# Optimization experiments

Hardware: AMD Instinct MI355X
Metric: run time of the kernel (lower is better)

## Reference

```python
import jax, jax.numpy as jnp
import numpy as np

B, L, K, NRBF = 2, 2048, 32, 16
NODE_F, EDGE_F = 128, 128
MAX_REL = 32  # af2 relpos -> 2*32+1 = 65 bins
NODE_IN, EDGE_IN = 21 + 6 + 8, 65 + 25 * NRBF + 1 + 2


def _ln(x, g, b, eps=1e-5):
    mu = jnp.mean(x, -1, keepdims=True)
    var = jnp.var(x, -1, keepdims=True)
    return (x - mu) / jnp.sqrt(var + eps) * g + b


def _normalize(t):
    return jnp.nan_to_num(t / jnp.linalg.norm(t, axis=-1, keepdims=True))


def _dihedral(p0, p1, p2, p3):
    u0, u1, u2 = p2 - p1, p0 - p1, p3 - p2
    n1 = _normalize(jnp.cross(u0, u1))
    n2 = _normalize(jnp.cross(u0, u2))
    sgn = jnp.sign(jnp.sum(jnp.cross(u1, u2) * u0, -1))
    return jnp.nan_to_num(sgn * jnp.arccos(jnp.sum(n1 * n2, -1)))


def setup_inputs() -> dict:
    key = jax.random.key(0)
    ks = jax.random.split(key, 9)
    return {
        "X": jax.random.normal(ks[0], (B, L, 4, 3), jnp.float32) * 5.0,
        "S": jax.random.randint(ks[1], (B, L), 0, 21),
        "BB_D_sincos": jax.random.normal(ks[2], (B, L, 3, 2), jnp.float32),
        "SC_D_sincos": jax.random.normal(ks[3], (B, L, 4, 2), jnp.float32),
        "chain_indices": jax.random.randint(ks[4], (B, L), 0, 2),
        "mask": jnp.ones((B, L), jnp.float32),
        "W_node": jax.random.normal(ks[5], (NODE_IN, NODE_F), jnp.float32) * 0.05,
        "b_node": jnp.zeros((NODE_F,), jnp.float32),
        "g_node": jnp.ones((NODE_F,), jnp.float32),
        "beta_node": jnp.zeros((NODE_F,), jnp.float32),
        "W_edge": jax.random.normal(ks[6], (EDGE_IN, EDGE_F), jnp.float32) * 0.05,
        "b_edge": jnp.zeros((EDGE_F,), jnp.float32),
        "g_edge": jnp.ones((EDGE_F,), jnp.float32),
        "beta_edge": jnp.zeros((EDGE_F,), jnp.float32),
    }


def reference(X, S, BB_D_sincos, SC_D_sincos, chain_indices, mask,
              W_node, b_node, g_node, beta_node,
              W_edge, b_edge, g_edge, beta_edge):
    Bn, Ln = X.shape[:2]
    N, Ca, C, O = X[:, :, 0], X[:, :, 1], X[:, :, 2], X[:, :, 3]
    # ---- masked pairwise Ca distances + kNN topk (smallest) ----
    m2 = mask[:, None, :] * mask[:, :, None]                      # [B,L,L]
    dX = Ca[:, :, None, :] - Ca[:, None, :, :]
    D = m2 * jnp.sqrt(jnp.sum(dX * dX, -1) + 1e-6)
    D_adj = D + 2.0 * (1.0 - m2) * jnp.max(D, -1, keepdims=True)
    _, E_idx = jax.lax.top_k(-D_adj, K)                           # [B,L,K]
    bidx = jnp.arange(Bn)[:, None, None]
    # ---- af2 relative-position one-hot (residue_index=None path) ----
    offset = E_idx - jnp.arange(Ln)[None, :, None]
    E_pos = jax.nn.one_hot(jnp.clip(offset + MAX_REL, 0, 2 * MAX_REL),
                           2 * MAX_REL + 1, dtype=jnp.float32)    # [B,L,K,65]
    # ---- impute CB, 5x5 atomic-distance RBFs at neighbors only ----
    bv, cv = Ca - N, C - Ca
    Cb = -0.58273431 * jnp.cross(bv, cv) + 0.56802827 * bv - 0.54067466 * cv + Ca
    X5 = jnp.stack((N, Ca, C, O, Cb), axis=-2)                    # [B,L,5,3]
    X5_nb = X5[bidx, E_idx]                                       # [B,L,K,5,3]
    dA = X5[:, :, None, :, None, :] - X5_nb[:, :, :, None, :, :]  # [B,L,K,5i,5j,3]
    Dn = jnp.sqrt(jnp.sum(dA * dA, -1) + 1e-6)                    # [B,L,K,5,5]
    mu = jnp.linspace(0.0, 20.0, NRBF)
    sigma = 20.0 / NRBF
    RBF_all = jnp.exp(-(((Dn[..., None] - mu) / sigma) ** 2))
    RBF_all = RBF_all.reshape(Bn, Ln, K, 25 * NRBF)               # i-major, j, rbf order
    # ---- edge type: same-chain indicator + 1 ----
    ch_nb = chain_indices[bidx, E_idx]
    E_type = ((ch_nb == chain_indices[:, :, None]).astype(jnp.float32) + 1.0)[..., None]
    # ---- pairwise dihedrals, evaluated only at neighbors ----
    N_nb, Ca_nb, C_nb = N[bidx, E_idx], Ca[bidx, E_idx], C[bidx, E_idx]
    ir_phi = _dihedral(C[:, :, None, :], N_nb, Ca_nb, C_nb)
    ir_psi = _dihedral(N[:, :, None, :], Ca[:, :, None, :], C[:, :, None, :], N_nb)
    dihed = jnp.stack((ir_phi, ir_psi), -1)                       # [B,L,K,2]
    # ---- fuse + embed ----
    E = jnp.concatenate((E_pos, RBF_all, E_type, dihed), -1)      # [B,L,K,468]
    V = jnp.concatenate((jax.nn.one_hot(S, 21, dtype=jnp.float32),
                         BB_D_sincos.reshape(Bn, Ln, -1),
                         SC_D_sincos.reshape(Bn, Ln, -1)), -1)    # [B,L,35]
    h_V = _ln(V @ W_node + b_node, g_node, beta_node)
    h_E = _ln(E @ W_edge + b_edge, g_edge, beta_edge)
    return (h_V, h_E, E_idx, X)
```

## Files before the change

### kernel.cpp

```cpp
#include <hip/hip_runtime.h>
#include <math.h>

#define NB 2
#define NL 2048
#define NK 32
#define NODE_F 128
#define EDGE_F 128

#define OFF_HV   0
#define OFF_HE   (NB*NL*NODE_F)
#define OFF_EIDX (OFF_HE + NB*NL*NK*EDGE_F)
#define OFF_X    (OFF_EIDX + NB*NL*NK)

#define ACH 7
#define BCH 6
#define SAW 232

typedef __attribute__((ext_vector_type(8))) short v8s;
typedef __attribute__((ext_vector_type(4))) float v4f;

__device__ __forceinline__ short f2bf(float f) {
    unsigned u = __float_as_uint(f);
    unsigned r = u + 0x7fffu + ((u >> 16) & 1u);
    return (short)(r >> 16);
}

#if __has_builtin(__builtin_amdgcn_exp2f)
#define EXP2F(x) __builtin_amdgcn_exp2f(x)
#else
#define EXP2F(x) __expf((x) * 0.6931471805599453f)
#endif

__device__ __forceinline__ unsigned bfpack(float f0, float f1) {
    unsigned u0 = __float_as_uint(f0), u1 = __float_as_uint(f1);
#if __has_builtin(__builtin_amdgcn_perm)
    return __builtin_amdgcn_perm(u1, u0, 0x07060302u);
#else
    return (u1 & 0xFFFF0000u) | (u0 >> 16);
#endif
}

template<int CTRL>
__device__ __forceinline__ unsigned long long dpp_min_step(unsigned long long x) {
    unsigned lo = (unsigned)x, hi = (unsigned)(x >> 32);
    unsigned plo = (unsigned)__builtin_amdgcn_update_dpp((int)lo, (int)lo, CTRL, 0xF, 0xF, false);
    unsigned phi = (unsigned)__builtin_amdgcn_update_dpp((int)hi, (int)hi, CTRL, 0xF, 0xF, false);
    unsigned long long p = (((unsigned long long)phi) << 32) | plo;
    return p < x ? p : x;
}
__device__ __forceinline__ unsigned long long wave_min_u64_dpp(unsigned long long x) {
    x = dpp_min_step<0xB1>(x);
    x = dpp_min_step<0x4E>(x);
    x = dpp_min_step<0x141>(x);
    x = dpp_min_step<0x140>(x);
    x = dpp_min_step<0x142>(x);
    x = dpp_min_step<0x143>(x);
    return x;
}

__device__ __forceinline__ void cross3(const float a[3], const float b[3], float c[3]) {
    c[0] = a[1]*b[2] - a[2]*b[1];
    c[1] = a[2]*b[0] - a[0]*b[2];
    c[2] = a[0]*b[1] - a[1]*b[0];
}
__device__ __forceinline__ float dot3(const float a[3], const float b[3]) {
    return a[0]*b[0] + a[1]*b[1] + a[2]*b[2];
}
__device__ float dihedral_f(const float p0[3], const float p1[3],
                            const float p2[3], const float p3[3]) {
    float u0[3], u1[3], u2[3];
    for (int d = 0; d < 3; d++) {
        u0[d] = p2[d] - p1[d];
        u1[d] = p0[d] - p1[d];
        u2[d] = p3[d] - p2[d];
    }
    float n1[3], n2[3], c12[3];
    cross3(u0, u1, n1);
    cross3(u0, u2, n2);
    cross3(u1, u2, c12);
    float l1 = sqrtf(dot3(n1, n1));
    float l2 = sqrtf(dot3(n2, n2));
    float cosang = dot3(n1, n2) / (l1 * l2);
    float s = dot3(c12, u0);
    float sgn = (s > 0.f) ? 1.f : ((s < 0.f) ? -1.f : 0.f);
    float r = sgn * acosf(cosang);
    return isnan(r) ? 0.f : r;
}

__global__ void prep_wconv_kernel(const float* __restrict__ X, float* __restrict__ X5,
                                  float* __restrict__ Cax, float* __restrict__ Cay,
                                  float* __restrict__ Caz, float* __restrict__ out,
                                  const float* __restrict__ We, const float* __restrict__ be,
                                  short* __restrict__ WTf) {
    int blk = blockIdx.x;
    if (blk < 16) {
        int row = blk * 256 + threadIdx.x;
        float v[12];
#pragma unroll
        for (int t = 0; t < 12; t++) v[t] = X[row * 12 + t];
#pragma unroll
        for (int t = 0; t < 12; t++) out[OFF_X + row * 12 + t] = v[t];
        Cax[row] = v[3]; Cay[row] = v[4]; Caz[row] = v[5];
        float bv[3], cv[3], cr[3];
        for (int d = 0; d < 3; d++) { bv[d] = v[3+d] - v[d]; cv[d] = v[6+d] - v[3+d]; }
        cross3(bv, cv, cr);
        float* x5 = X5 + row * 15;
#pragma unroll
        for (int t = 0; t < 12; t++) x5[t] = v[t];
        for (int d = 0; d < 3; d++)
            x5[12 + d] = -0.58273431f * cr[d] + 0.56802827f * bv[d] - 0.54067466f * cv[d] + v[3+d];
    } else {
        int t = (blk - 16) * 256 + threadIdx.x;
        if (t >= 13 * 8 * 64) return;
        int lane = t & 63;
        int nt = (t >> 6) & 7;
        int ch = t >> 9;
        int n = nt * 16 + (lane & 15);
        int kbase = ch * 32 + (lane >> 4) * 8;
        short* dst = WTf + (size_t)t * 8;
#pragma unroll
        for (int j = 0; j < 8; j++) {
            int k = kbase + j;
            float f;
            if (k < 403) f = We[(65 + k) * 128 + n];
            else if (k == 403) f = be[n];
            else f = 0.f;
            dst[j] = f2bf(f);
        }
    }
}

#define KNN_QMIN(Q) {                                                                  \
    unsigned long long a_ = key[(Q)*8+0] < key[(Q)*8+1] ? key[(Q)*8+0] : key[(Q)*8+1]; \
    unsigned long long b_ = key[(Q)*8+2] < key[(Q)*8+3] ? key[(Q)*8+2] : key[(Q)*8+3]; \
    unsigned long long c_ = key[(Q)*8+4] < key[(Q)*8+5] ? key[(Q)*8+4] : key[(Q)*8+5]; \
    unsigned long long d_ = key[(Q)*8+6] < key[(Q)*8+7] ? key[(Q)*8+6] : key[(Q)*8+7]; \
    a_ = a_ < b_ ? a_ : b_; c_ = c_ < d_ ? c_ : d_;                                    \
    qm[(Q)] = a_ < c_ ? a_ : c_; }

#define KNN_STEP(Q) {                                                                  \
    _Pragma("unroll")                                                                  \
    for (int i_ = 0; i_ < 8; i_++)                                                     \
        key[(Q)*8+i_] = (me && tstar == (Q)*8+i_) ? ~0ull : key[(Q)*8+i_];             \
    KNN_QMIN(Q) }

__global__ __launch_bounds__(256) void knn_node_kernel(const float* __restrict__ Cax,
                                                       const float* __restrict__ Cay,
                                                       const float* __restrict__ Caz,
                                                       const float* __restrict__ mask,
                                                       const int* __restrict__ S,
                                                       const float* __restrict__ BB,
                                                       const float* __restrict__ SC,
                                                       const float* __restrict__ Wn,
                                                       const float* __restrict__ bn,
                                                       const float* __restrict__ gn,
                                                       const float* __restrict__ betan,
                                                       int* __restrict__ EidxW,
                                                       float* __restrict__ out) {
    int tid = threadIdx.x;
    int w = tid >> 6, l = tid & 63;
    int row = blockIdx.x * 4 + w;

    {
        int f0 = l, f1 = 64 + l;
        int s = S[row];
        float a0 = bn[f0] + Wn[s * NODE_F + f0];
        float a1 = bn[f1] + Wn[s * NODE_F + f1];
#pragma unroll
        for (int t = 0; t < 6; t++) {
            float x = BB[row * 6 + t];
            a0 += x * Wn[(21 + t) * NODE_F + f0];
            a1 += x * Wn[(21 + t) * NODE_F + f1];
        }
#pragma unroll
        for (int t = 0; t < 8; t++) {
            float x = SC[row * 8 + t];
            a0 += x * Wn[(27 + t) * NODE_F + f0];
            a1 += x * Wn[(27 + t) * NODE_F + f1];
        }
        float sm = a0 + a1;
#pragma unroll
        for (int st = 1; st < 64; st <<= 1) sm += __shfl_xor(sm, st, 64);
        float mean = sm * (1.0f / 128.0f);
        float d0 = a0 - mean, d1 = a1 - mean;
        float q = d0 * d0 + d1 * d1;
#pragma unroll
        for (int st = 1; st < 64; st <<= 1) q += __shfl_xor(q, st, 64);
        float rstd = 1.0f / sqrtf(q * (1.0f / 128.0f) + 1e-5f);
        out[OFF_HV + row * NODE_F + f0] = d0 * rstd * gn[f0] + betan[f0];
        out[OFF_HV + row * NODE_F + f1] = d1 * rstd * gn[f1] + betan[f1];
    }

    int b = row / NL;
    int base = b * NL;
    const float* mrow = mask + base;

    float cx = Cax[row], cy = Cay[row], cz = Caz[row];
    float mi = mrow[row - base];

    float K[32];
    float lmax = 0.0f;
#pragma unroll
    for (int t = 0; t < 32; t++) {
        int j = t * 64 + l;
        float dx = __fsub_rn(cx, Cax[base + j]);
        float dy = __fsub_rn(cy, Cay[base + j]);
        float dz = __fsub_rn(cz, Caz[base + j]);
        float ss = __fadd_rn(__fadd_rn(__fadd_rn(__fmul_rn(dx, dx), __fmul_rn(dy, dy)),
                                       __fmul_rn(dz, dz)), 1e-6f);
        float d = __fmul_rn(__fmul_rn(mi, mrow[j]), __fsqrt_rn(ss));
        K[t] = d;
        lmax = fmaxf(lmax, d);
    }
#pragma unroll
    for (int s = 1; s < 64; s <<= 1) lmax = fmaxf(lmax, __shfl_xor(lmax, s, 64));
#pragma unroll
    for (int t = 0; t < 32; t++) {
        int j = t * 64 + l;
        float m2 = __fmul_rn(mi, mrow[j]);
        K[t] = __fadd_rn(K[t], __fmul_rn(__fmul_rn(2.0f, __fsub_rn(1.0f, m2)), lmax));
    }

    unsigned long long key[32];
#pragma unroll
    for (int t = 0; t < 32; t++)
        key[t] = (((unsigned long long)__float_as_uint(K[t])) << 32) | (unsigned)(t * 64 + l);

    unsigned long long qm[4];
    KNN_QMIN(0) KNN_QMIN(1) KNN_QMIN(2) KNN_QMIN(3)

    int selj = 0;
#pragma unroll 1
    for (int r = 0; r < NK; r++) {
        unsigned long long m01 = qm[0] < qm[1] ? qm[0] : qm[1];
        unsigned long long m23 = qm[2] < qm[3] ? qm[2] : qm[3];
        unsigned long long g = m01 < m23 ? m01 : m23;
        g = wave_min_u64_dpp(g);
        unsigned j = (unsigned)__builtin_amdgcn_readlane((int)(unsigned)g, 63);
        if (l == r) selj = (int)j;
        bool me = ((j & 63u) == (unsigned)l);
        int tstar = (int)(j >> 6);
        switch (tstar >> 3) {
            case 0: KNN_STEP(0) break;
            case 1: KNN_STEP(1) break;
            case 2: KNN_STEP(2) break;
            default: KNN_STEP(3) break;
        }
    }
    if (l < NK) {
        EidxW[row * NK + l] = selj;
        out[OFF_EIDX + row * NK + l] = (float)selj;
    }
}

__global__ __launch_bounds__(256, 4) void edge7_kernel(const float* __restrict__ X5,
                                                       const int* __restrict__ Eidx,
                                                       const int* __restrict__ chain,
                                                       const float* __restrict__ We,
                                                       const float* __restrict__ ge,
                                                       const float* __restrict__ betae,
                                                       const short* __restrict__ WTf,
                                                       float* __restrict__ out) {
    __shared__ short sA[64 * SAW];
    __shared__ float sXj[64][17];
    __shared__ float sXi[2][15];
    __shared__ float sRow[2][128];
    __shared__ int   sJ[64];
    __shared__ int   sPos[64];
    __shared__ float sEt[64], sPhi[64], sPsi[64];

    int tid = threadIdx.x;
    int e0 = blockIdx.x * 64;
    int b = e0 / (NL * NK);
    int i0 = (e0 / NK) % NL;
    int lane = tid & 63, w = tid >> 6;

    if (tid < 64) sJ[tid] = Eidx[e0 + tid];
    if (tid < 30) sXi[tid / 15][tid % 15] = X5[(b * NL + i0 + tid / 15) * 15 + (tid % 15)];
    if (tid >= 128 && tid < 128 + 128) {
        int n2 = tid - 128;
        sRow[0][n2] = ge[n2];
        sRow[1][n2] = betae[n2];
    }
    __syncthreads();

    for (int t = tid; t < 64 * 15; t += 256) {
        int e = t / 15, c2 = t % 15;
        sXj[e][c2] = X5[(b * NL + sJ[e]) * 15 + c2];
    }
    if (tid < 64) {
        int e = tid;
        int i = i0 + (e >> 5);
        int j = sJ[e];
        int off = j - i + 32;
        off = off < 0 ? 0 : (off > 64 ? 64 : off);
        sPos[e] = off;
        sEt[e] = (chain[b * NL + j] == chain[b * NL + i]) ? 2.0f : 1.0f;
    }
    __syncthreads();

    if (tid < 128) {
        int e = tid & 63;
        const float* xi = sXi[e >> 5];
        const float* xj = sXj[e];
        if (tid < 64) sPhi[e] = dihedral_f(&xi[6], &xj[0], &xj[3], &xj[6]);
        else          sPsi[e] = dihedral_f(&xi[0], &xi[3], &xi[6], &xj[0]);
    }

    const float Ac = -0.92332482616893658f;
    int eg_ = w * 16 + (lane & 15);
    int q_ = lane >> 4;
    const float* xiG = sXi[eg_ >> 5];
    const float* xjG = sXj[eg_];
    short* rowp = sA + eg_ * SAW;
    float hfq = (float)(q_ & 1);

#define GEN_A(hh, CNT)                                                         \
    {                                                                          \
        _Pragma("unroll")                                                      \
        for (int t = 0; t < (CNT); t++) {                                      \
            int o = q_ + t * 4;                                                \
            int kg = (hh) * 224 + o * 8;                                       \
            int pair = kg >> 4;                                                \
            union { unsigned u[4]; v8s v; } au;                                \
            if (pair >= 25) {                                                  \
                if ((hh) == 1 && o == 22) {         \
                    au.u[0] = bfpack(sEt[eg_], sPhi[eg_]);                     \
                    au.u[1] = bfpack(sPsi[eg_], 1.0f);                         \
                    au.u[2] = 0; au.u[3] = 0;                                  \
                } else {                                                       \
                    au.u[0] = 0; au.u[1] = 0; au.u[2] = 0; au.u[3] = 0;        \
                }                                                              \
            } else {                                                           \
                int a = pair / 5, cc = pair - a * 5;                           \
                float dx = xiG[a*3+0] - xjG[cc*3+0];                           \
                float dy = xiG[a*3+1] - xjG[cc*3+1];                           \
                float dz = xiG[a*3+2] - xjG[cc*3+2];                           \
                float d = sqrtf(dx*dx + dy*dy + dz*dz + 1e-6f);                \
                float ee = __fmaf_rn(hfq, -10.666666666666666f, d);            \
                float t1 = Ac * ee * ee;                                       \
                _Pragma("unroll")                                              \
                for (int jp = 0; jp < 4; jp++) {                               \
                    const float mu0 = (float)(2 * jp) * (20.0f / 15.0f);       \
                    const float mu1 = (float)(2 * jp + 1) * (20.0f / 15.0f);   \
                    const float B0 = -2.0f * Ac * mu0, C0 = Ac * mu0 * mu0;    \
                    const float B1 = -2.0f * Ac * mu1, C1 = Ac * mu1 * mu1;    \
                    float r0 = EXP2F(__fmaf_rn(B0, ee, t1) + C0);              \
                    float r1 = EXP2F(__fmaf_rn(B1, ee, t1) + C1);              \
                    au.u[jp] = bfpack(r0, r1);                                 \
                }                                                              \
            }                                                                  \
            *(v8s*)(rowp + o * 8) = au.v;                                      \
        }                                                                      \
    }

    GEN_A(0, ACH)
    __syncthreads();

    int cl = lane & 15, kq = lane >> 4;
    int ntA = 2 * w, ntB = ntA + 1;
    const char* sAc = (const char*)sA;
    int abase0 = cl * (SAW * 2) + kq * 16;

    v4f acc[4][2];
#pragma unroll
    for (int eg = 0; eg < 4; eg++) { acc[eg][0] = (v4f){0.f,0.f,0.f,0.f}; acc[eg][1] = (v4f){0.f,0.f,0.f,0.f}; }

#define MMA_HALF(CHBASE, CNT)                                                  \
    {                                                                          \
        _Pragma("unroll 2")                                                    \
        for (int chl = 0; chl < (CNT); chl++) {                                \
            const v8s* gb = (const v8s*)WTf + ((size_t)((CHBASE) + chl) * 512 + lane); \
            v8s b0 = gb[ntA * 64];                                             \
            v8s b1 = gb[ntB * 64];                                             \
            int ab = abase0 + chl * 64;                                        \
            v8s a0 = *(const v8s*)(sAc + ab);                                  \
            v8s a1 = *(const v8s*)(sAc + ab + 16 * (SAW * 2));                 \
            v8s a2 = *(const v8s*)(sAc + ab + 32 * (SAW * 2));                 \
            v8s a3 = *(const v8s*)(sAc + ab + 48 * (SAW * 2));                 \
            acc[0][0] = __builtin_amdgcn_mfma_f32_16x16x32_bf16(a0, b0, acc[0][0], 0, 0, 0); \
            acc[0][1] = __builtin_amdgcn_mfma_f32_16x16x32_bf16(a0, b1, acc[0][1], 0, 0, 0); \
            acc[1][0] = __builtin_amdgcn_mfma_f32_16x16x32_bf16(a1, b0, acc[1][0], 0, 0, 0); \
            acc[1][1] = __builtin_amdgcn_mfma_f32_16x16x32_bf16(a1, b1, acc[1][1], 0, 0, 0); \
            acc[2][0] = __builtin_amdgcn_mfma_f32_16x16x32_bf16(a2, b0, acc[2][0], 0, 0, 0); \
            acc[2][1] = __builtin_amdgcn_mfma_f32_16x16x32_bf16(a2, b1, acc[2][1], 0, 0, 0); \
            acc[3][0] = __builtin_amdgcn_mfma_f32_16x16x32_bf16(a3, b0, acc[3][0], 0, 0, 0); \
            acc[3][1] = __builtin_amdgcn_mfma_f32_16x16x32_bf16(a3, b1, acc[3][1], 0, 0, 0); \
        }                                                                      \
    }

    MMA_HALF(0, ACH)
    __syncthreads();
    GEN_A(1, BCH)
    __syncthreads();
    MMA_HALF(ACH, BCH)

    float2* sRed = (float2*)&sXj[0][0];
    int nA = ntA * 16 + cl, nB = nA + 16;
    float r4A = sRow[0][nA], r5A = sRow[1][nA];
    float r4B = sRow[0][nB], r5B = sRow[1][nB];

#pragma unroll
    for (int eg = 0; eg < 4; eg++) {
#pragma unroll
        for (int r = 0; r < 4; r++) {
            int e = eg * 16 + kq * 4 + r;
            int pos = sPos[e];
            float v0 = acc[eg][0][r] + We[pos * 128 + nA];
            float v1 = acc[eg][1][r] + We[pos * 128 + nB];
            acc[eg][0][r] = v0; acc[eg][1][r] = v1;
            float s = v0 + v1, q2 = v0 * v0 + v1 * v1;
#pragma unroll
            for (int s2 = 1; s2 < 16; s2 <<= 1) {
                s  += __shfl_xor(s,  s2, 64);
                q2 += __shfl_xor(q2, s2, 64);
            }
            if (cl == 0) sRed[e * 4 + w] = make_float2(s, q2);
        }
    }
    __syncthreads();

#pragma unroll
    for (int eg = 0; eg < 4; eg++) {
#pragma unroll
        for (int r = 0; r < 4; r++) {
            int e = eg * 16 + kq * 4 + r;
            float4 pa = *(const float4*)&sRed[e * 4];
            float4 pb = *(const float4*)&sRed[e * 4 + 2];
            float s  = pa.x + pa.z + pb.x + pb.z;
            float q2 = pa.y + pa.w + pb.y + pb.w;
            float mean = s * (1.0f / 128.0f);
            float var = q2 * (1.0f / 128.0f) - mean * mean;
            float rstd = rsqrtf(var + 1e-5f);
            size_t base = OFF_HE + (size_t)(e0 + e) * 128;
            out[base + nA] = (acc[eg][0][r] - mean) * rstd * r4A + r5A;
            out[base + nB] = (acc[eg][1][r] - mean) * rstd * r4B + r5B;
        }
    }
}

extern "C" void kernel_launch(void* const* d_in, const int* in_sizes, int n_in,
                              void* d_out, int out_size, void* d_ws, size_t ws_size,
                              hipStream_t stream) {
    (void)in_sizes; (void)n_in; (void)out_size; (void)ws_size;
    const float* X    = (const float*)d_in[0];
    const int*   S    = (const int*)d_in[1];
    const float* BB   = (const float*)d_in[2];
    const float* SC   = (const float*)d_in[3];
    const int*   chain= (const int*)d_in[4];
    const float* mask = (const float*)d_in[5];
    const float* Wn   = (const float*)d_in[6];
    const float* bn   = (const float*)d_in[7];
    const float* gn   = (const float*)d_in[8];
    const float* betan= (const float*)d_in[9];
    const float* We   = (const float*)d_in[10];
    const float* be   = (const float*)d_in[11];
    const float* ge   = (const float*)d_in[12];
    const float* betae= (const float*)d_in[13];
    float* out = (float*)d_out;

    char* ws = (char*)d_ws;
    int*   EidxW = (int*)ws;
    float* X5    = (float*)(ws + 524288);
    short* WTf   = (short*)(ws + 770048);
    float* Cax   = (float*)(ws + 876544);
    float* Cay   = (float*)(ws + 892928);
    float* Caz   = (float*)(ws + 909312);

    hipLaunchKernelGGL(prep_wconv_kernel, dim3(16 + 26), dim3(256), 0, stream,
                       X, X5, Cax, Cay, Caz, out, We, be, WTf);
    hipLaunchKernelGGL(knn_node_kernel, dim3(NB * NL / 4), dim3(256), 0, stream,
                       Cax, Cay, Caz, mask, S, BB, SC, Wn, bn, gn, betan, EidxW, out);
    hipLaunchKernelGGL(edge7_kernel, dim3(NB * NL * NK / 64), dim3(256), 0, stream,
                       X5, EidxW, chain, We, ge, betae, WTf, out);
}
```

Baseline: 184.9 us.

## Fuse prep into kNN kernel with LDS Ca staging; RBF via exp recurrence

Merges the prep/weight-conversion kernel into the kNN/node kernel: the extra blocks do the X copy, X5 build and weight packing, and kNN blocks stage Ca coordinates in shared memory straight from X. This removes one launch and the Cax/Cay/Caz workspace round trip. Separately, the edge kernel's 8 RBF exponentials per pair are replaced by two exp2 calls plus a multiplicative recurrence, with ee clamped to avoid overflow. The recurrence may lose some precision in the bf16-packed RBF values, and the LDS staging is repeated in each of the 1024 kNN blocks.

```diff
diff --git a/kernel.cpp b/kernel.cpp
--- a/kernel.cpp
+++ b/kernel.cpp
@@ -87,49 +87,6 @@
     return isnan(r) ? 0.f : r;
 }
 
-__global__ void prep_wconv_kernel(const float* __restrict__ X, float* __restrict__ X5,
-                                  float* __restrict__ Cax, float* __restrict__ Cay,
-                                  float* __restrict__ Caz, float* __restrict__ out,
-                                  const float* __restrict__ We, const float* __restrict__ be,
-                                  short* __restrict__ WTf) {
-    int blk = blockIdx.x;
-    if (blk < 16) {
-        int row = blk * 256 + threadIdx.x;
-        float v[12];
-#pragma unroll
-        for (int t = 0; t < 12; t++) v[t] = X[row * 12 + t];
-#pragma unroll
-        for (int t = 0; t < 12; t++) out[OFF_X + row * 12 + t] = v[t];
-        Cax[row] = v[3]; Cay[row] = v[4]; Caz[row] = v[5];
-        float bv[3], cv[3], cr[3];
-        for (int d = 0; d < 3; d++) { bv[d] = v[3+d] - v[d]; cv[d] = v[6+d] - v[3+d]; }
-        cross3(bv, cv, cr);
-        float* x5 = X5 + row * 15;
-#pragma unroll
-        for (int t = 0; t < 12; t++) x5[t] = v[t];
-        for (int d = 0; d < 3; d++)
-            x5[12 + d] = -0.58273431f * cr[d] + 0.56802827f * bv[d] - 0.54067466f * cv[d] + v[3+d];
-    } else {
-        int t = (blk - 16) * 256 + threadIdx.x;
-        if (t >= 13 * 8 * 64) return;
-        int lane = t & 63;
-        int nt = (t >> 6) & 7;
-        int ch = t >> 9;
-        int n = nt * 16 + (lane & 15);
-        int kbase = ch * 32 + (lane >> 4) * 8;
-        short* dst = WTf + (size_t)t * 8;
-#pragma unroll
-        for (int j = 0; j < 8; j++) {
-            int k = kbase + j;
-            float f;
-            if (k < 403) f = We[(65 + k) * 128 + n];
-            else if (k == 403) f = be[n];
-            else f = 0.f;
-            dst[j] = f2bf(f);
-        }
-    }
-}
-
 #define KNN_QMIN(Q) {                                                                  \
     unsigned long long a_ = key[(Q)*8+0] < key[(Q)*8+1] ? key[(Q)*8+0] : key[(Q)*8+1]; \
     unsigned long long b_ = key[(Q)*8+2] < key[(Q)*8+3] ? key[(Q)*8+2] : key[(Q)*8+3]; \
@@ -144,22 +101,74 @@
         key[(Q)*8+i_] = (me && tstar == (Q)*8+i_) ? ~0ull : key[(Q)*8+i_];             \
     KNN_QMIN(Q) }
 
-__global__ __launch_bounds__(256) void knn_node_kernel(const float* __restrict__ Cax,
-                                                       const float* __restrict__ Cay,
-                                                       const float* __restrict__ Caz,
-                                                       const float* __restrict__ mask,
-                                                       const int* __restrict__ S,
-                                                       const float* __restrict__ BB,
-                                                       const float* __restrict__ SC,
-                                                       const float* __restrict__ Wn,
-                                                       const float* __restrict__ bn,
-                                                       const float* __restrict__ gn,
-                                                       const float* __restrict__ betan,
-                                                       int* __restrict__ EidxW,
-                                                       float* __restrict__ out) {
+__global__ __launch_bounds__(256) void fused_pre_kernel(const float* __restrict__ X,
+                                                        const float* __restrict__ mask,
+                                                        const int* __restrict__ S,
+                                                        const float* __restrict__ BB,
+                                                        const float* __restrict__ SC,
+                                                        const float* __restrict__ Wn,
+                                                        const float* __restrict__ bn,
+                                                        const float* __restrict__ gn,
+                                                        const float* __restrict__ betan,
+                                                        const float* __restrict__ We,
+                                                        const float* __restrict__ be,
+                                                        float* __restrict__ X5,
+                                                        short* __restrict__ WTf,
+                                                        int* __restrict__ EidxW,
+                                                        float* __restrict__ out) {
+    __shared__ float sCa[NL * 3];
+    int blk = blockIdx.x;
     int tid = threadIdx.x;
+
+    if (blk >= 1024) {
+        if (blk < 1040) {
+            int row = (blk - 1024) * 256 + tid;
+            float v[12];
+#pragma unroll
+            for (int t = 0; t < 12; t++) v[t] = X[row * 12 + t];
+#pragma unroll
+            for (int t = 0; t < 12; t++) out[OFF_X + row * 12 + t] = v[t];
+            float bv[3], cv[3], cr[3];
+            for (int d = 0; d < 3; d++) { bv[d] = v[3+d] - v[d]; cv[d] = v[6+d] - v[3+d]; }
+            cross3(bv, cv, cr);
+            float* x5 = X5 + row * 15;
+#pragma unroll
+            for (int t = 0; t < 12; t++) x5[t] = v[t];
+            for (int d = 0; d < 3; d++)
+                x5[12 + d] = -0.58273431f * cr[d] + 0.56802827f * bv[d] - 0.54067466f * cv[d] + v[3+d];
+        } else {
+            int t = (blk - 1040) * 256 + tid;
+            if (t >= 13 * 8 * 64) return;
+            int lane = t & 63;
+            int nt = (t >> 6) & 7;
+            int ch = t >> 9;
+            int n = nt * 16 + (lane & 15);
+            int kbase = ch * 32 + (lane >> 4) * 8;
+            short* dst = WTf + (size_t)t * 8;
+#pragma unroll
+            for (int j = 0; j < 8; j++) {
+                int k = kbase + j;
+                float f;
+                if (k < 403) f = We[(65 + k) * 128 + n];
+                else if (k == 403) f = be[n];
+                else f = 0.f;
+                dst[j] = f2bf(f);
+            }
+        }
+        return;
+    }
+
     int w = tid >> 6, l = tid & 63;
-    int row = blockIdx.x * 4 + w;
+    int row = blk * 4 + w;
+    int b = row / NL;
+    int base = b * NL;
+
+    for (int idx = tid; idx < NL; idx += 256) {
+        const float* xp = X + (size_t)(base + idx) * 12 + 3;
+        sCa[idx * 3 + 0] = xp[0];
+        sCa[idx * 3 + 1] = xp[1];
+        sCa[idx * 3 + 2] = xp[2];
+    }
 
     {
         int f0 = l, f1 = 64 + l;
@@ -190,22 +199,21 @@
         out[OFF_HV + row * NODE_F + f0] = d0 * rstd * gn[f0] + betan[f0];
         out[OFF_HV + row * NODE_F + f1] = d1 * rstd * gn[f1] + betan[f1];
     }
-
-    int b = row / NL;
-    int base = b * NL;
+    __syncthreads();
+
     const float* mrow = mask + base;
-
-    float cx = Cax[row], cy = Cay[row], cz = Caz[row];
-    float mi = mrow[row - base];
+    int lrow = row - base;
+    float cx = sCa[lrow * 3 + 0], cy = sCa[lrow * 3 + 1], cz = sCa[lrow * 3 + 2];
+    float mi = mrow[lrow];
 
     float K[32];
     float lmax = 0.0f;
 #pragma unroll
     for (int t = 0; t < 32; t++) {
         int j = t * 64 + l;
-        float dx = __fsub_rn(cx, Cax[base + j]);
-        float dy = __fsub_rn(cy, Cay[base + j]);
-        float dz = __fsub_rn(cz, Caz[base + j]);
+        float dx = __fsub_rn(cx, sCa[j * 3 + 0]);
+        float dy = __fsub_rn(cy, sCa[j * 3 + 1]);
+        float dz = __fsub_rn(cz, sCa[j * 3 + 2]);
         float ss = __fadd_rn(__fadd_rn(__fadd_rn(__fmul_rn(dx, dx), __fmul_rn(dy, dy)),
                                        __fmul_rn(dz, dz)), 1e-6f);
         float d = __fmul_rn(__fmul_rn(mi, mrow[j]), __fsqrt_rn(ss));
@@ -253,7 +261,7 @@
     }
 }
 
-__global__ __launch_bounds__(256, 4) void edge7_kernel(const float* __restrict__ X5,
+__global__ __launch_bounds__(256, 4) void edge8_kernel(const float* __restrict__ X5,
                                                        const int* __restrict__ Eidx,
                                                        const int* __restrict__ chain,
                                                        const float* __restrict__ We,
@@ -307,7 +315,10 @@
         else          sPsi[e] = dihedral_f(&xi[0], &xi[3], &xi[6], &xj[0]);
     }
 
-    const float Ac = -0.92332482616893658f;
+    const float Ac  = -0.92332482616893658f;
+    const float K1c = 2.46219953645049755f;
+    const float Rc  = EXP2F(-1.64146635763366503f);
+    const float R2c = Rc * Rc;
     int eg_ = w * 16 + (lane & 15);
     int q_ = lane >> 4;
     const float* xiG = sXi[eg_ >> 5];
@@ -337,18 +348,20 @@
                 float dy = xiG[a*3+1] - xjG[cc*3+1];                           \
                 float dz = xiG[a*3+2] - xjG[cc*3+2];                           \
                 float d = sqrtf(dx*dx + dy*dy + dz*dz + 1e-6f);                \
-                float ee = __fmaf_rn(hfq, -10.666666666666666f, d);            \
-                float t1 = Ac * ee * ee;                                       \
-                _Pragma("unroll")                                              \
-                for (int jp = 0; jp < 4; jp++) {                               \
-                    const float mu0 = (float)(2 * jp) * (20.0f / 15.0f);       \
-                    const float mu1 = (float)(2 * jp + 1) * (20.0f / 15.0f);   \
-                    const float B0 = -2.0f * Ac * mu0, C0 = Ac * mu0 * mu0;    \
-                    const float B1 = -2.0f * Ac * mu1, C1 = Ac * mu1 * mu1;    \
-                    float r0 = EXP2F(__fmaf_rn(B0, ee, t1) + C0);              \
-                    float r1 = EXP2F(__fmaf_rn(B1, ee, t1) + C1);              \
-                    au.u[jp] = bfpack(r0, r1);                                 \
-                }                                                              \
+                float ee = fminf(__fmaf_rn(hfq, -10.666666666666666f, d), 40.f); \
+                float r0 = EXP2F(Ac * ee * ee);                                \
+                float g  = EXP2F(K1c * ee) * Rc;                               \
+                float r1 = r0 * g; g *= R2c;                                   \
+                float r2 = r1 * g; g *= R2c;                                   \
+                float r3 = r2 * g; g *= R2c;                                   \
+                float r4 = r3 * g; g *= R2c;                                   \
+                float r5 = r4 * g; g *= R2c;                                   \
+                float r6 = r5 * g; g *= R2c;                                   \
+                float r7 = r6 * g;                                             \
+                au.u[0] = bfpack(r0, r1);                                      \
+                au.u[1] = bfpack(r2, r3);                                      \
+                au.u[2] = bfpack(r4, r5);                                      \
+                au.u[3] = bfpack(r6, r7);                                      \
             }                                                                  \
             *(v8s*)(rowp + o * 8) = au.v;                                      \
         }                                                                      \
@@ -463,14 +476,10 @@
     int*   EidxW = (int*)ws;
     float* X5    = (float*)(ws + 524288);
     short* WTf   = (short*)(ws + 770048);
-    float* Cax   = (float*)(ws + 876544);
-    float* Cay   = (float*)(ws + 892928);
-    float* Caz   = (float*)(ws + 909312);
-
-    hipLaunchKernelGGL(prep_wconv_kernel, dim3(16 + 26), dim3(256), 0, stream,
-                       X, X5, Cax, Cay, Caz, out, We, be, WTf);
-    hipLaunchKernelGGL(knn_node_kernel, dim3(NB * NL / 4), dim3(256), 0, stream,
-                       Cax, Cay, Caz, mask, S, BB, SC, Wn, bn, gn, betan, EidxW, out);
-    hipLaunchKernelGGL(edge7_kernel, dim3(NB * NL * NK / 64), dim3(256), 0, stream,
+
+    hipLaunchKernelGGL(fused_pre_kernel, dim3(1024 + 16 + 26), dim3(256), 0, stream,
+                       X, mask, S, BB, SC, Wn, bn, gn, betan, We, be,
+                       X5, WTf, EidxW, out);
+    hipLaunchKernelGGL(edge8_kernel, dim3(NB * NL * NK / 64), dim3(256), 0, stream,
                        X5, EidxW, chain, We, ge, betae, WTf, out);
 }
```

Result: no change. 182.0 us (-1.5%).
